# Performance work log

Hardware: AMD Instinct MI355X
Metric: run time of the kernel (lower is better)

## Reference

```python
import jax, jax.numpy as jnp
import numpy as np

HEADS = 16
HIDDEN = 1024
D_HEAD = HIDDEN // HEADS
SCALE = float(D_HEAD) ** 0.5


def setup_inputs() -> dict:
    key = jax.random.key(0)
    ks = jax.random.split(key, 11)
    B, L = 2, 2048
    x = jax.random.normal(ks[0], (B, L, HIDDEN), dtype=jnp.float32)
    # 0/1 padding mask, broadcast over heads and query positions
    mask = jax.random.randint(ks[1], (B, 1, 1, L), 0, 2).astype(jnp.float32)
    s = 1.0 / np.sqrt(HIDDEN)
    Wq = jax.random.normal(ks[2], (HIDDEN, HIDDEN), dtype=jnp.float32) * s
    bq = jax.random.normal(ks[3], (HIDDEN,), dtype=jnp.float32) * s
    Wk = jax.random.normal(ks[4], (HIDDEN, HIDDEN), dtype=jnp.float32) * s
    bk = jax.random.normal(ks[5], (HIDDEN,), dtype=jnp.float32) * s
    Wv = jax.random.normal(ks[6], (HIDDEN, HIDDEN), dtype=jnp.float32) * s
    bv = jax.random.normal(ks[7], (HIDDEN,), dtype=jnp.float32) * s
    Wo = jax.random.normal(ks[8], (HIDDEN, HIDDEN), dtype=jnp.float32) * s
    bo = jax.random.normal(ks[9], (HIDDEN,), dtype=jnp.float32) * s
    return {"x": x, "mask": mask, "Wq": Wq, "bq": bq, "Wk": Wk, "bk": bk,
            "Wv": Wv, "bv": bv, "Wo": Wo, "bo": bo}


def reference(x, mask, Wq, bq, Wk, bk, Wv, bv, Wo, bo):
    B, L, _ = x.shape
    # projections (Linear: x @ W + b), split heads -> [B, H, L, Dh]
    def proj(W, b):
        return (jnp.dot(x, W) + b).reshape(B, L, HEADS, D_HEAD).transpose(0, 2, 1, 3)
    q = proj(Wq, bq)
    k = proj(Wk, bk)
    v = proj(Wv, bv)
    # scaled dot-product with additive mask: scores [B, H, Lq, Lk]
    scores = jnp.einsum('bhqd,bhkd->bhqk', q, k) / SCALE + mask * (-10000.0)
    attn = jax.nn.softmax(scores, axis=-1)  # dropout p=0.0 -> identity
    out = jnp.einsum('bhqk,bhkd->bhqd', attn, v)
    out = out.transpose(0, 2, 1, 3).reshape(B, L, HIDDEN)
    return jnp.dot(out, Wo) + bo
```

## Files before the change

kernel.cpp:

```cpp
#include <hip/hip_runtime.h>
#include <math.h>

typedef unsigned short u16;
typedef short v8s __attribute__((ext_vector_type(8)));
typedef float v4f __attribute__((ext_vector_type(4)));
typedef float v16f __attribute__((ext_vector_type(16)));

#define HIDDEN 1024
#define L_SEQ 2048
#define NH 16
#define DH 64
#define NKMAX 1280

#define QSCALE 0.18033688011112042f

__device__ __forceinline__ u16 f2bf(float f) {
  union { float f; unsigned int i; } c; c.f = f;
  unsigned int x = c.i;
  unsigned int r = (x + 0x7fffu + ((x >> 16) & 1u)) >> 16;
  return (u16)r;
}

#if defined(__has_builtin)
#if __has_builtin(__builtin_amdgcn_cvt_pk_bf16_f32)
#define HAS_PKBF 1
#endif
#if __has_builtin(__builtin_amdgcn_exp2f)
#define EXP2(x) __builtin_amdgcn_exp2f(x)
#endif
#if __has_builtin(__builtin_amdgcn_rcpf)
#define RCP(x) __builtin_amdgcn_rcpf(x)
#endif
#endif
#ifndef EXP2
#define EXP2(x) exp2f(x)
#endif
#ifndef RCP
#define RCP(x) (1.0f / (x))
#endif

__device__ __forceinline__ unsigned pkbf(float a, float b) {
#ifdef HAS_PKBF
  typedef __bf16 v2bf __attribute__((ext_vector_type(2)));
  union { v2bf v; unsigned u; } c;
  c.v = __builtin_amdgcn_cvt_pk_bf16_f32(a, b);
  return c.u;
#else
  return (unsigned)f2bf(a) | ((unsigned)f2bf(b) << 16);
#endif
}

__device__ __forceinline__ void gload16(const void* g, void* l) {
  void* gg = const_cast<void*>(g);
  __builtin_amdgcn_global_load_lds(
      (__attribute__((address_space(1))) void*)gg,
      (__attribute__((address_space(3))) void*)l, 16, 0, 0);
}

__device__ __forceinline__ v16f vzero16() {
  v16f z;
#pragma unroll
  for (int i = 0; i < 16; ++i) z[i] = 0.f;
  return z;
}

__global__ __launch_bounds__(256) void prep(
    const float* __restrict__ x, u16* __restrict__ xb,
    const float* __restrict__ Wq, const float* __restrict__ Wk,
    const float* __restrict__ Wv, const float* __restrict__ Wo,
    u16* __restrict__ WtQ, u16* __restrict__ WtK,
    u16* __restrict__ WtV, u16* __restrict__ WtO,
    const float* __restrict__ maskg, u16* __restrict__ keep,
    unsigned* __restrict__ nkslot) {
  const int bid = blockIdx.x;
  const int t = threadIdx.x;

  if (bid < 2048) {
    const int i = (bid * 256 + t) * 8;
    const float4 a = *(const float4*)(x + i);
    const float4 b = *(const float4*)(x + i + 4);
    unsigned o[4] = {pkbf(a.x, a.y), pkbf(a.z, a.w), pkbf(b.x, b.y), pkbf(b.z, b.w)};
    *(uint4*)(xb + i) = *(const uint4*)o;
    return;
  }

  if (bid < 6144) {
    const int m = bid - 2048;
    const int z = m >> 10;
    const int rem = m & 1023;
    const int bx = rem & 31, by = rem >> 5;
    const float* src; u16* dst;
    if (z == 0) { src = Wq; dst = WtQ; }
    else if (z == 1) { src = Wk; dst = WtK; }
    else if (z == 2) { src = Wv; dst = WtV; }
    else { src = Wo; dst = WtO; }

    __shared__ u16 tile[32][33];
    const int tx = t & 31, ty = t >> 5;
    const int xcol = bx * 32 + tx;
    const int y0 = by * 32;
#pragma unroll
    for (int i = ty; i < 32; i += 8)
      tile[i][tx] = f2bf(src[(size_t)(y0 + i) * HIDDEN + xcol]);
    __syncthreads();
    const int xo = y0 + tx;
#pragma unroll
    for (int i = ty; i < 32; i += 8)
      dst[(size_t)(bx * 32 + i) * HIDDEN + xo] = tile[tx][i];
    return;
  }

  if (t < 64) {
    const int b = bid - 6144;
    const int lane = t;
    const float* mp = maskg + b * L_SEQ;
    int cnt = 0;
#pragma unroll 1
    for (int j = 0; j < 32; ++j) cnt += (mp[lane * 32 + j] == 0.0f) ? 1 : 0;
    int inc = cnt;
#pragma unroll
    for (int off = 1; off < 64; off <<= 1) {
      const int v = __shfl_up(inc, off, 64);
      if (lane >= off) inc += v;
    }
    int base = inc - cnt;
    u16* kp = keep + b * L_SEQ;
#pragma unroll 1
    for (int j = 0; j < 32; ++j) {
      const int k = lane * 32 + j;
      if (mp[k] == 0.0f) kp[base++] = (u16)k;
    }
    const int total = __shfl(inc, 63, 64);
    for (int i = total + lane; i < NKMAX; i += 64) kp[i] = 0;
    if (lane == 0) nkslot[b] = (unsigned)total;
  }
}

__global__ __launch_bounds__(256) void gemm128(
    const u16* __restrict__ A,
    const u16* __restrict__ B0, const u16* __restrict__ B1, const u16* __restrict__ B2,
    const float* __restrict__ bias0, const float* __restrict__ bias1, const float* __restrict__ bias2,
    u16* __restrict__ C0, u16* __restrict__ C1, u16* __restrict__ C2,
    float* __restrict__ Cf, const u16* __restrict__ keep,
    const unsigned* __restrict__ nkslot,
    int qkv_mode) {
  __shared__ __align__(16) u16 As[128 * 32];
  __shared__ __align__(16) u16 Bs[128 * 32];

  const u16* Bt; const float* bias; u16* C;
  if (blockIdx.z == 0) { Bt = B0; bias = bias0; C = C0; }
  else if (blockIdx.z == 1) { Bt = B1; bias = bias1; C = C1; }
  else { Bt = B2; bias = bias2; C = C2; }
  const int mode = qkv_mode ? (blockIdx.z == 0 ? 1 : (blockIdx.z == 1 ? 2 : 3)) : 0;
  const float oscale = (mode == 1) ? QSCALE : 1.0f;

  const int t = threadIdx.x;
  const int lane = t & 63;
  const int wave = t >> 6;
  const int quad = lane >> 4;
  const int l16 = lane & 15;
  const int wm = wave >> 1;
  const int wn = wave & 1;

  const int n0 = blockIdx.x * 128;
  const int sr = t >> 2;
  const int sc = (t & 3) * 8;

  int m0 = blockIdx.y * 128;
  int kvb = 0;
  const u16* Ag0;
  const u16* Ag1;
  if (mode == 2 || mode == 3) {
    const int y = blockIdx.y;
    if (y >= 20) return;
    kvb = y / 10;
    m0 = (y % 10) * 128;
    const unsigned nk = nkslot[kvb];
    if ((unsigned)m0 >= ((nk + 63u) & ~63u)) return;
    const int sr0 = keep[kvb * L_SEQ + m0 + sr];
    const int sr1 = keep[kvb * L_SEQ + m0 + 64 + sr];
    Ag0 = A + ((size_t)(kvb * L_SEQ + sr0)) * HIDDEN + sc;
    Ag1 = A + ((size_t)(kvb * L_SEQ + sr1)) * HIDDEN + sc;
  } else {
    Ag0 = A + (size_t)(m0 + sr) * HIDDEN + sc;
    Ag1 = Ag0 + (size_t)64 * HIDDEN;
  }
  const u16* Bg0 = Bt + (size_t)(n0 + sr) * HIDDEN + sc;
  const u16* Bg1 = Bg0 + (size_t)64 * HIDDEN;
  u16* Al0 = &As[sr * 32 + sc];
  u16* Al1 = &As[(64 + sr) * 32 + sc];
  u16* Bl0 = &Bs[sr * 32 + sc];
  u16* Bl1 = &Bs[(64 + sr) * 32 + sc];

  v4f acc[4][4];
#pragma unroll
  for (int mi = 0; mi < 4; ++mi)
#pragma unroll
    for (int ni = 0; ni < 4; ++ni)
      acc[mi][ni] = (v4f){0.f, 0.f, 0.f, 0.f};

  for (int k0 = 0; k0 < HIDDEN; k0 += 32) {
    __syncthreads();
    gload16(Ag0 + k0, Al0);
    gload16(Ag1 + k0, Al1);
    gload16(Bg0 + k0, Bl0);
    gload16(Bg1 + k0, Bl1);
    __syncthreads();

    v8s a[4], b[4];
#pragma unroll
    for (int mi = 0; mi < 4; ++mi)
      a[mi] = *(const v8s*)&As[(wm * 64 + mi * 16 + l16) * 32 + quad * 8];
#pragma unroll
    for (int ni = 0; ni < 4; ++ni)
      b[ni] = *(const v8s*)&Bs[(wn * 64 + ni * 16 + l16) * 32 + quad * 8];
#pragma unroll
    for (int mi = 0; mi < 4; ++mi)
#pragma unroll
      for (int ni = 0; ni < 4; ++ni)
        acc[mi][ni] = __builtin_amdgcn_mfma_f32_16x16x32_bf16(a[mi], b[ni], acc[mi][ni], 0, 0, 0);
  }

#pragma unroll
  for (int ni = 0; ni < 4; ++ni) {
    const int col = n0 + wn * 64 + ni * 16 + l16;
    const float bv = bias[col];
#pragma unroll
    for (int mi = 0; mi < 4; ++mi) {
      const int row0 = m0 + wm * 64 + mi * 16 + quad * 4;
      const float v0 = (acc[mi][ni][0] + bv) * oscale;
      const float v1 = (acc[mi][ni][1] + bv) * oscale;
      const float v2 = (acc[mi][ni][2] + bv) * oscale;
      const float v3 = (acc[mi][ni][3] + bv) * oscale;
      if (mode == 0) {
        Cf[(size_t)(row0 + 0) * HIDDEN + col] = v0;
        Cf[(size_t)(row0 + 1) * HIDDEN + col] = v1;
        Cf[(size_t)(row0 + 2) * HIDDEN + col] = v2;
        Cf[(size_t)(row0 + 3) * HIDDEN + col] = v3;
      } else if (mode == 1) {
        const int hh = col >> 6, d = col & 63;
        const float vv[4] = {v0, v1, v2, v3};
#pragma unroll
        for (int i = 0; i < 4; ++i) {
          const int rr = row0 + i;
          const int bb = rr >> 11, l = rr & 2047;
          C[((size_t)(bb * NH + hh) * L_SEQ + l) * DH + d] = f2bf(vv[i]);
        }
      } else if (mode == 2) {
        const int hh = col >> 6, d = col & 63;
        const float vv[4] = {v0, v1, v2, v3};
#pragma unroll
        for (int i = 0; i < 4; ++i)
          C[((size_t)(kvb * NH + hh) * L_SEQ + row0 + i) * DH + d] = f2bf(vv[i]);
      } else {
        const int hh = col >> 6, d = col & 63;
        unsigned pk[2] = {pkbf(v0, v1), pkbf(v2, v3)};
        *(uint2*)&C[((size_t)((kvb * NH + hh) * DH + d)) * L_SEQ + row0] = *(const uint2*)pk;
      }
    }
  }
}


#define MKPF(dst, P0, P1, P2, P3, P4, P5, P6, P7)                   \
  {                                                                 \
    const unsigned a_ = pkbf(P0, P1), c_ = pkbf(P2, P3);            \
    const unsigned b_ = pkbf(P4, P5), d_ = pkbf(P6, P7);            \
    const unsigned a2_ = (unsigned)__shfl((int)a_, lane ^ 32, 64);  \
    const unsigned b2_ = (unsigned)__shfl((int)b_, lane ^ 32, 64);  \
    const unsigned c2_ = (unsigned)__shfl((int)c_, lane ^ 32, 64);  \
    const unsigned d2_ = (unsigned)__shfl((int)d_, lane ^ 32, 64);  \
    union { unsigned u[4]; v8s v; } f_;                             \
    f_.u[0] = lo32 ? a_ : b2_;                                      \
    f_.u[1] = lo32 ? c_ : d2_;                                      \
    f_.u[2] = lo32 ? a2_ : b_;                                      \
    f_.u[3] = lo32 ? c2_ : d_;                                      \
    dst = f_.v;                                                     \
  }

__global__ __launch_bounds__(512) void attn256(
    const u16* __restrict__ Qg, const u16* __restrict__ Kcg, const u16* __restrict__ VTg,
    const unsigned* __restrict__ nkslot, u16* __restrict__ Og) {
  __shared__ __align__(16) u16 lds[16384];

  const int t = threadIdx.x;
  const int lane = t & 63;
  const int w = t >> 6;
  const int l31 = lane & 31;
  const int hi = lane >> 5;
  const bool lo32 = lane < 32;
  const int e7 = l31 & 7;

  const int bid = blockIdx.x;
  const int bh = bid & 31;
  const int q0 = (bid >> 5) * 256;
  const int b = bh >> 4;
  const int h = bh & 15;

  const size_t base = (size_t)bh * L_SEQ * DH;
  const u16* Qp = Qg + base;
  const u16* Kp = Kcg + base;
  const u16* VTp = VTg + base;

  const int nkb = (int)nkslot[b];
  const int ntiles = (nkb + 63) >> 6;

  const int r8 = lane >> 3;
  const int sl = lane & 7;
  const int og8 = (sl ^ r8) * 8;
  const int koff = (w * 8 + r8) * DH + og8;
  const int voff = (w * 8 + r8) * L_SEQ + og8;
  u16* const kdst = &lds[(w * 8) * 64];
  u16* const vdst = &lds[8192 + (w * 8) * 64];

  gload16(Kp + koff, kdst);
  gload16(VTp + voff, vdst);

  const int qrow = q0 + w * 32 + l31;
  v8s qf[4];
#pragma unroll
  for (int dc = 0; dc < 4; ++dc)
    qf[dc] = *(const v8s*)&Qp[(size_t)qrow * DH + dc * 16 + hi * 8];

  v16f oacc0 = vzero16(), oacc1 = vzero16();
  float lsum = 0.f;

  for (int n = 0; n < ntiles; ++n) {
    __syncthreads();
    const int ksb = (n & 1) * 4096;
    const int vtb = 8192 + (n & 1) * 4096;
    if (n + 1 < ntiles) {
      const int k1 = (n + 1) * 64;
      const int ksb2 = ((n + 1) & 1) * 4096;
      const int vtb2 = ((n + 1) & 1) * 4096;
      gload16(Kp + (size_t)k1 * DH + koff, kdst + ksb2);
      gload16(VTp + voff + k1, vdst + vtb2);
    }

    v16f s0 = vzero16(), s1 = vzero16();
    __builtin_amdgcn_s_setprio(1);
#pragma unroll
    for (int dc = 0; dc < 4; ++dc) {
      const int po = ((dc * 2 + hi) ^ e7) * 8;
      const v8s kf0 = *(const v8s*)&lds[ksb + l31 * 64 + po];
      const v8s kf1 = *(const v8s*)&lds[ksb + (32 + l31) * 64 + po];
      s0 = __builtin_amdgcn_mfma_f32_32x32x16_bf16(kf0, qf[dc], s0, 0, 0, 0);
      s1 = __builtin_amdgcn_mfma_f32_32x32x16_bf16(kf1, qf[dc], s1, 0, 0, 0);
    }
    __builtin_amdgcn_s_setprio(0);

    const int kb0 = n * 64;
    float p[32];
#pragma unroll
    for (int r = 0; r < 16; ++r) {
      p[r]      = EXP2(s0[r]);
      p[16 + r] = EXP2(s1[r]);
    }
    if (kb0 + 64 > nkb) {
#pragma unroll
      for (int r = 0; r < 16; ++r) {
        const int kk = kb0 + (r & 3) + 8 * (r >> 2) + 4 * hi;
        if (kk >= nkb) p[r] = 0.f;
        if (kk + 32 >= nkb) p[16 + r] = 0.f;
      }
    }
    {
      float a0 = 0.f, a1 = 0.f, a2 = 0.f, a3 = 0.f;
#pragma unroll
      for (int r = 0; r < 8; ++r) {
        a0 += p[r]; a1 += p[8 + r]; a2 += p[16 + r]; a3 += p[24 + r];
      }
      lsum += (a0 + a1) + (a2 + a3);
    }

    v8s pf0, pf1, pf2, pf3;
    MKPF(pf0, p[0],  p[1],  p[2],  p[3],  p[4],  p[5],  p[6],  p[7]);
    MKPF(pf1, p[8],  p[9],  p[10], p[11], p[12], p[13], p[14], p[15]);
    MKPF(pf2, p[16], p[17], p[18], p[19], p[20], p[21], p[22], p[23]);
    MKPF(pf3, p[24], p[25], p[26], p[27], p[28], p[29], p[30], p[31]);

    __builtin_amdgcn_s_setprio(1);
#pragma unroll
    for (int kc = 0; kc < 4; ++kc) {
      const v8s pb = (kc == 0) ? pf0 : (kc == 1) ? pf1 : (kc == 2) ? pf2 : pf3;
      const int po = ((kc * 2 + hi) ^ e7) * 8;
      const v8s vf0 = *(const v8s*)&lds[vtb + l31 * 64 + po];
      const v8s vf1 = *(const v8s*)&lds[vtb + (32 + l31) * 64 + po];
      oacc0 = __builtin_amdgcn_mfma_f32_32x32x16_bf16(vf0, pb, oacc0, 0, 0, 0);
      oacc1 = __builtin_amdgcn_mfma_f32_32x32x16_bf16(vf1, pb, oacc1, 0, 0, 0);
    }
    __builtin_amdgcn_s_setprio(0);
  }

  const float ltot = lsum + __shfl(lsum, lane ^ 32, 64);
  const float linv = RCP(ltot);

  const size_t ob = ((size_t)(b * L_SEQ + qrow)) * HIDDEN + h * DH;
#pragma unroll
  for (int r = 0; r < 16; r += 2) {
    const int d0 = (r & 3) + 8 * (r >> 2) + 4 * hi;
    const unsigned w0 = pkbf(oacc0[r] * linv, oacc0[r + 1] * linv);
    const unsigned w1 = pkbf(oacc1[r] * linv, oacc1[r + 1] * linv);
    *(unsigned*)&Og[ob + d0] = w0;
    *(unsigned*)&Og[ob + 32 + d0] = w1;
  }
}

extern "C" void kernel_launch(void* const* d_in, const int* in_sizes, int n_in,
                              void* d_out, int out_size, void* d_ws, size_t ws_size,
                              hipStream_t stream) {
  const float* x    = (const float*)d_in[0];
  const float* mask = (const float*)d_in[1];
  const float* Wq   = (const float*)d_in[2];
  const float* bq   = (const float*)d_in[3];
  const float* Wk   = (const float*)d_in[4];
  const float* bk   = (const float*)d_in[5];
  const float* Wv   = (const float*)d_in[6];
  const float* bv   = (const float*)d_in[7];
  const float* Wo   = (const float*)d_in[8];
  const float* bo   = (const float*)d_in[9];
  float* out = (float*)d_out;
  u16* ws = (u16*)d_ws;

  const unsigned M1 = 1u << 20;
  u16* WtQ = ws;
  u16* WtK = ws + M1;
  u16* WtV = ws + 2 * M1;
  u16* WtO = ws + 3 * M1;
  u16* xb  = ws + 4 * M1;
  u16* Qb  = ws + 8 * M1;
  u16* Kc  = ws + 12 * M1;
  u16* VTc = ws + 16 * M1;
  u16* Ob  = ws + 20 * M1;
  u16* keep = ws + 16 * M1 - 8192;
  unsigned* nkslot = (unsigned*)(ws + 16 * M1 - 8192 - 8);

  prep<<<6146, 256, 0, stream>>>(x, xb, Wq, Wk, Wv, Wo, WtQ, WtK, WtV, WtO,
                                 mask, keep, nkslot);
  gemm128<<<dim3(8, 32, 3), 256, 0, stream>>>(xb, WtQ, WtK, WtV, bq, bk, bv,
                                              Qb, Kc, VTc, nullptr, keep, nkslot, 1);
  attn256<<<dim3(256), 512, 0, stream>>>(Qb, Kc, VTc, nkslot, Ob);
  gemm128<<<dim3(8, 32, 1), 256, 0, stream>>>(Ob, WtO, WtO, WtO, bo, bo, bo,
                                              nullptr, nullptr, nullptr, out, nullptr, nullptr, 0);
}
```

Measured before the change: 189.5 us.

## Double attention K/V tile to 128 keys and use permlane32 swap for P

The attention kernel now stages 128 keys per iteration instead of 64, which doubles the LDS buffers to 64 KB and halves the number of barriers and prefetch rounds. Each 128-key tile is processed as two 64-key halves, with a new swizzled layout for the 128-wide V^T rows. The cross-half-wave exchange that builds the P operand now uses v_permlane32_swap instead of four __shfl calls plus selects. The larger LDS footprint may reduce occupancy, and padding waste grows when the valid key count is not a multiple of 128.

New measurement: 185.4 us. 2.1% less time.

```diff
diff --git a/kernel.cpp b/kernel.cpp
--- a/kernel.cpp
+++ b/kernel.cpp
@@ -262,33 +262,34 @@
 }
 
 
-#define MKPF(dst, P0, P1, P2, P3, P4, P5, P6, P7)                   \
-  {                                                                 \
-    const unsigned a_ = pkbf(P0, P1), c_ = pkbf(P2, P3);            \
-    const unsigned b_ = pkbf(P4, P5), d_ = pkbf(P6, P7);            \
-    const unsigned a2_ = (unsigned)__shfl((int)a_, lane ^ 32, 64);  \
-    const unsigned b2_ = (unsigned)__shfl((int)b_, lane ^ 32, 64);  \
-    const unsigned c2_ = (unsigned)__shfl((int)c_, lane ^ 32, 64);  \
-    const unsigned d2_ = (unsigned)__shfl((int)d_, lane ^ 32, 64);  \
-    union { unsigned u[4]; v8s v; } f_;                             \
-    f_.u[0] = lo32 ? a_ : b2_;                                      \
-    f_.u[1] = lo32 ? c_ : d2_;                                      \
-    f_.u[2] = lo32 ? a2_ : b_;                                      \
-    f_.u[3] = lo32 ? c2_ : d_;                                      \
-    dst = f_.v;                                                     \
-  }
-
-__global__ __launch_bounds__(512) void attn256(
+#define XCH(D0_, D2_, A_, B_)                                        \
+  {                                                                  \
+    unsigned a_ = (A_), b_ = (B_);                                   \
+    asm("v_permlane32_swap_b32 %0, %1" : "+v"(a_), "+v"(b_));        \
+    D0_ = a_;                                      \
+    D2_ = b_;                                      \
+  }
+
+#define MKPF(dst, P0, P1, P2, P3, P4, P5, P6, P7)                    \
+  {                                                                  \
+    const unsigned A_ = pkbf(P0, P1), C_ = pkbf(P2, P3);             \
+    const unsigned B_ = pkbf(P4, P5), D_ = pkbf(P6, P7);             \
+    union { unsigned u[4]; v8s v; } f_;                              \
+    XCH(f_.u[0], f_.u[2], A_, B_);                                   \
+    XCH(f_.u[1], f_.u[3], C_, D_);                                   \
+    dst = f_.v;                                                      \
+  }
+
+__global__ __launch_bounds__(512) void attn512(
     const u16* __restrict__ Qg, const u16* __restrict__ Kcg, const u16* __restrict__ VTg,
     const unsigned* __restrict__ nkslot, u16* __restrict__ Og) {
-  __shared__ __align__(16) u16 lds[16384];
+  __shared__ __align__(16) u16 lds[32768];
 
   const int t = threadIdx.x;
   const int lane = t & 63;
   const int w = t >> 6;
   const int l31 = lane & 31;
   const int hi = lane >> 5;
-  const bool lo32 = lane < 32;
   const int e7 = l31 & 7;
 
   const int bid = blockIdx.x;
@@ -303,18 +304,20 @@
   const u16* VTp = VTg + base;
 
   const int nkb = (int)nkslot[b];
-  const int ntiles = (nkb + 63) >> 6;
-
-  const int r8 = lane >> 3;
-  const int sl = lane & 7;
-  const int og8 = (sl ^ r8) * 8;
-  const int koff = (w * 8 + r8) * DH + og8;
-  const int voff = (w * 8 + r8) * L_SEQ + og8;
-  u16* const kdst = &lds[(w * 8) * 64];
-  u16* const vdst = &lds[8192 + (w * 8) * 64];
-
-  gload16(Kp + koff, kdst);
-  gload16(VTp + voff, vdst);
+  const int ntiles = (nkb + 127) >> 7;
+
+  const int r8 = lane >> 3, sl8 = lane & 7;
+  const int koff = (w * 8 + r8) * DH + (sl8 ^ r8) * 8;
+  const int r4 = lane >> 4, sl16 = lane & 15;
+  const int vrow = w * 4 + r4;
+  const int voff = vrow * L_SEQ + ((((sl16 & 7) ^ (vrow & 7)) | (sl16 & 8)) * 8);
+  u16* const kd = &lds[(w * 8) * 64];
+  u16* const vd = &lds[16384 + (w * 4) * 128];
+
+  gload16(Kp + koff, kd);
+  gload16(Kp + 64 * DH + koff, kd + 64 * 64);
+  gload16(VTp + voff, vd);
+  gload16(VTp + 32 * L_SEQ + voff, vd + 32 * 128);
 
   const int qrow = q0 + w * 32 + l31;
   v8s qf[4];
@@ -327,69 +330,75 @@
 
   for (int n = 0; n < ntiles; ++n) {
     __syncthreads();
-    const int ksb = (n & 1) * 4096;
-    const int vtb = 8192 + (n & 1) * 4096;
+    const int ksb = (n & 1) * 8192;
+    const int vtb = 16384 + (n & 1) * 8192;
     if (n + 1 < ntiles) {
-      const int k1 = (n + 1) * 64;
-      const int ksb2 = ((n + 1) & 1) * 4096;
-      const int vtb2 = ((n + 1) & 1) * 4096;
-      gload16(Kp + (size_t)k1 * DH + koff, kdst + ksb2);
-      gload16(VTp + voff + k1, vdst + vtb2);
+      const size_t k1 = (size_t)(n + 1) * 128;
+      const int s2 = ((n + 1) & 1) * 8192;
+      gload16(Kp + k1 * DH + koff, kd + s2);
+      gload16(Kp + (k1 + 64) * DH + koff, kd + s2 + 64 * 64);
+      gload16(VTp + k1 + voff, vd + s2);
+      gload16(VTp + k1 + 32 * L_SEQ + voff, vd + s2 + 32 * 128);
     }
 
-    v16f s0 = vzero16(), s1 = vzero16();
-    __builtin_amdgcn_s_setprio(1);
-#pragma unroll
-    for (int dc = 0; dc < 4; ++dc) {
-      const int po = ((dc * 2 + hi) ^ e7) * 8;
-      const v8s kf0 = *(const v8s*)&lds[ksb + l31 * 64 + po];
-      const v8s kf1 = *(const v8s*)&lds[ksb + (32 + l31) * 64 + po];
-      s0 = __builtin_amdgcn_mfma_f32_32x32x16_bf16(kf0, qf[dc], s0, 0, 0, 0);
-      s1 = __builtin_amdgcn_mfma_f32_32x32x16_bf16(kf1, qf[dc], s1, 0, 0, 0);
+    const int kb0 = n * 128;
+#pragma unroll
+    for (int h2 = 0; h2 < 2; ++h2) {
+      v16f s0 = vzero16(), s1 = vzero16();
+      __builtin_amdgcn_s_setprio(1);
+#pragma unroll
+      for (int dc = 0; dc < 4; ++dc) {
+        const int po = ((dc * 2 + hi) ^ e7) * 8;
+        const v8s kf0 = *(const v8s*)&lds[ksb + (h2 * 64 + l31) * 64 + po];
+        const v8s kf1 = *(const v8s*)&lds[ksb + (h2 * 64 + 32 + l31) * 64 + po];
+        s0 = __builtin_amdgcn_mfma_f32_32x32x16_bf16(kf0, qf[dc], s0, 0, 0, 0);
+        s1 = __builtin_amdgcn_mfma_f32_32x32x16_bf16(kf1, qf[dc], s1, 0, 0, 0);
+      }
+      __builtin_amdgcn_s_setprio(0);
+
+      const int kh0 = kb0 + h2 * 64;
+      float p[32];
+#pragma unroll
+      for (int r = 0; r < 16; ++r) {
+        p[r]      = EXP2(s0[r]);
+        p[16 + r] = EXP2(s1[r]);
+      }
+      if (kh0 + 64 > nkb) {
+#pragma unroll
+        for (int r = 0; r < 16; ++r) {
+          const int kk = kh0 + (r & 3) + 8 * (r >> 2) + 4 * hi;
+          if (kk >= nkb) p[r] = 0.f;
+          if (kk + 32 >= nkb) p[16 + r] = 0.f;
+        }
+      }
+      {
+        float a0 = 0.f, a1 = 0.f, a2 = 0.f, a3 = 0.f;
+#pragma unroll
+        for (int r = 0; r < 8; ++r) {
+          a0 += p[r]; a1 += p[8 + r]; a2 += p[16 + r]; a3 += p[24 + r];
+        }
+        lsum += (a0 + a1) + (a2 + a3);
+      }
+
+      v8s pf0, pf1, pf2, pf3;
+      MKPF(pf0, p[0],  p[1],  p[2],  p[3],  p[4],  p[5],  p[6],  p[7]);
+      MKPF(pf1, p[8],  p[9],  p[10], p[11], p[12], p[13], p[14], p[15]);
+      MKPF(pf2, p[16], p[17], p[18], p[19], p[20], p[21], p[22], p[23]);
+      MKPF(pf3, p[24], p[25], p[26], p[27], p[28], p[29], p[30], p[31]);
+
+      __builtin_amdgcn_s_setprio(1);
+#pragma unroll
+      for (int kc = 0; kc < 4; ++kc) {
+        const v8s pb = (kc == 0) ? pf0 : (kc == 1) ? pf1 : (kc == 2) ? pf2 : pf3;
+        const int oc = h2 * 8 + kc * 2 + hi;
+        const int po = (((oc & 7) ^ e7) | (oc & 8)) * 8;
+        const v8s vf0 = *(const v8s*)&lds[vtb + l31 * 128 + po];
+        const v8s vf1 = *(const v8s*)&lds[vtb + (32 + l31) * 128 + po];
+        oacc0 = __builtin_amdgcn_mfma_f32_32x32x16_bf16(vf0, pb, oacc0, 0, 0, 0);
+        oacc1 = __builtin_amdgcn_mfma_f32_32x32x16_bf16(vf1, pb, oacc1, 0, 0, 0);
+      }
+      __builtin_amdgcn_s_setprio(0);
     }
-    __builtin_amdgcn_s_setprio(0);
-
-    const int kb0 = n * 64;
-    float p[32];
-#pragma unroll
-    for (int r = 0; r < 16; ++r) {
-      p[r]      = EXP2(s0[r]);
-      p[16 + r] = EXP2(s1[r]);
-    }
-    if (kb0 + 64 > nkb) {
-#pragma unroll
-      for (int r = 0; r < 16; ++r) {
-        const int kk = kb0 + (r & 3) + 8 * (r >> 2) + 4 * hi;
-        if (kk >= nkb) p[r] = 0.f;
-        if (kk + 32 >= nkb) p[16 + r] = 0.f;
-      }
-    }
-    {
-      float a0 = 0.f, a1 = 0.f, a2 = 0.f, a3 = 0.f;
-#pragma unroll
-      for (int r = 0; r < 8; ++r) {
-        a0 += p[r]; a1 += p[8 + r]; a2 += p[16 + r]; a3 += p[24 + r];
-      }
-      lsum += (a0 + a1) + (a2 + a3);
-    }
-
-    v8s pf0, pf1, pf2, pf3;
-    MKPF(pf0, p[0],  p[1],  p[2],  p[3],  p[4],  p[5],  p[6],  p[7]);
-    MKPF(pf1, p[8],  p[9],  p[10], p[11], p[12], p[13], p[14], p[15]);
-    MKPF(pf2, p[16], p[17], p[18], p[19], p[20], p[21], p[22], p[23]);
-    MKPF(pf3, p[24], p[25], p[26], p[27], p[28], p[29], p[30], p[31]);
-
-    __builtin_amdgcn_s_setprio(1);
-#pragma unroll
-    for (int kc = 0; kc < 4; ++kc) {
-      const v8s pb = (kc == 0) ? pf0 : (kc == 1) ? pf1 : (kc == 2) ? pf2 : pf3;
-      const int po = ((kc * 2 + hi) ^ e7) * 8;
-      const v8s vf0 = *(const v8s*)&lds[vtb + l31 * 64 + po];
-      const v8s vf1 = *(const v8s*)&lds[vtb + (32 + l31) * 64 + po];
-      oacc0 = __builtin_amdgcn_mfma_f32_32x32x16_bf16(vf0, pb, oacc0, 0, 0, 0);
-      oacc1 = __builtin_amdgcn_mfma_f32_32x32x16_bf16(vf1, pb, oacc1, 0, 0, 0);
-    }
-    __builtin_amdgcn_s_setprio(0);
   }
 
   const float ltot = lsum + __shfl(lsum, lane ^ 32, 64);
@@ -439,7 +448,7 @@
                                  mask, keep, nkslot);
   gemm128<<<dim3(8, 32, 3), 256, 0, stream>>>(xb, WtQ, WtK, WtV, bq, bk, bv,
                                               Qb, Kc, VTc, nullptr, keep, nkslot, 1);
-  attn256<<<dim3(256), 512, 0, stream>>>(Qb, Kc, VTc, nkslot, Ob);
+  attn512<<<dim3(256), 512, 0, stream>>>(Qb, Kc, VTc, nkslot, Ob);
   gemm128<<<dim3(8, 32, 1), 256, 0, stream>>>(Ob, WtO, WtO, WtO, bo, bo, bo,
                                               nullptr, nullptr, nullptr, out, nullptr, nullptr, 0);
 }
```
